# Kernel tuning notes

Hardware: AMD Instinct MI355X
Metric: run time of the kernel (lower is better)

The kernel has to match this reference:

```python
import jax, jax.numpy as jnp
import numpy as np

D_MODEL = 2048
N_HEADS = 16
D_HEAD = D_MODEL // N_HEADS


def setup_inputs() -> dict:
    key = jax.random.key(0)
    ks = jax.random.split(key, 9)
    s = 1.0 / np.sqrt(D_MODEL)
    x = jax.random.normal(ks[0], (2, 2048, D_MODEL), dtype=jnp.float32)
    wq = jax.random.uniform(ks[1], (D_MODEL, D_MODEL), jnp.float32, -s, s)
    wk = jax.random.uniform(ks[2], (D_MODEL, D_MODEL), jnp.float32, -s, s)
    wv = jax.random.uniform(ks[3], (D_MODEL, D_MODEL), jnp.float32, -s, s)
    wo = jax.random.uniform(ks[4], (D_MODEL, D_MODEL), jnp.float32, -s, s)
    bq = jax.random.uniform(ks[5], (D_MODEL,), jnp.float32, -s, s)
    bk = jax.random.uniform(ks[6], (D_MODEL,), jnp.float32, -s, s)
    bv = jax.random.uniform(ks[7], (D_MODEL,), jnp.float32, -s, s)
    bo = jax.random.uniform(ks[8], (D_MODEL,), jnp.float32, -s, s)
    return {"x": x, "wq": wq, "bq": bq, "wk": wk, "bk": bk,
            "wv": wv, "bv": bv, "wo": wo, "bo": bo}


def reference(x, wq, bq, wk, bk, wv, bv, wo, bo):
    b, s, _ = x.shape
    # torch Linear: y = x @ W.T + b
    q = (jnp.einsum('bsd,ed->bse', x, wq) + bq).reshape(b, s, N_HEADS, D_HEAD)
    k = (jnp.einsum('bsd,ed->bse', x, wk) + bk).reshape(b, s, N_HEADS, D_HEAD)
    v = (jnp.einsum('bsd,ed->bse', x, wv) + bv).reshape(b, s, N_HEADS, D_HEAD)
    scale = 1.0 / np.sqrt(D_HEAD).astype(np.float32)
    # [b, h, s, s] attention scores (naive full materialization, as in source)
    attn = jnp.einsum('bqhd,bkhd->bhqk', q, k) * scale
    attn = jax.nn.softmax(attn, axis=-1)
    out = jnp.einsum('bhqk,bkhd->bqhd', attn, v).reshape(b, s, D_MODEL)
    return jnp.einsum('bsd,ed->bse', out, wo) + bo
```

## Files before the change

kernel.cpp:

```cpp
#include <hip/hip_runtime.h>

#define D_MODEL 2048
#define SEQ     2048
#define NB      2
#define NH      16
#define DH      128
#define MROWS   (NB*SEQ)
#define GK      2048
#define NT      (GK/64)

typedef __bf16 bf16x8 __attribute__((ext_vector_type(8)));
typedef float  f32x4  __attribute__((ext_vector_type(4)));
typedef unsigned short ushort8 __attribute__((ext_vector_type(8)));
typedef unsigned int   u32x4   __attribute__((ext_vector_type(4)));

__device__ __forceinline__ unsigned short f2bf(float f) {
  unsigned int u = __float_as_uint(f);
  u += 0x7FFFu + ((u >> 16) & 1u);
  return (unsigned short)(u >> 16);
}

__device__ __forceinline__ unsigned int cvtpk_bf16(float lo, float hi) {
  unsigned int r;
  asm("v_cvt_pk_bf16_f32 %0, %1, %2" : "=v"(r) : "v"(lo), "v"(hi));
  return r;
}

__device__ __forceinline__ void gload16(void* lds, const void* g) {
  __builtin_amdgcn_global_load_lds(
      (__attribute__((address_space(1))) void*)(g),
      (__attribute__((address_space(3))) void*)(lds), 16, 0, 0);
}

__global__ __launch_bounds__(256) void cast_f32_bf16(
    const float* __restrict__ in, unsigned short* __restrict__ out) {
  int i = blockIdx.x * 256 + threadIdx.x;
  const float4* p = (const float4*)in;
  float4 a = p[2*i], b = p[2*i+1];
  ushort8 o;
  o[0]=f2bf(a.x); o[1]=f2bf(a.y); o[2]=f2bf(a.z); o[3]=f2bf(a.w);
  o[4]=f2bf(b.x); o[5]=f2bf(b.y); o[6]=f2bf(b.z); o[7]=f2bf(b.w);
  ((ushort8*)out)[i] = o;
}

__global__ __launch_bounds__(512, 2) void gemm256(
    const unsigned short* __restrict__ A,
    const unsigned short* __restrict__ B,
    const float* __restrict__ b0, const float* __restrict__ b1,
    const float* __restrict__ b2,
    unsigned short* __restrict__ qo, unsigned short* __restrict__ ko,
    unsigned short* __restrict__ vo, float* __restrict__ fo,
    int mode, int nblk)
{
  __shared__ char lds[3*49152];

  const int tid  = threadIdx.x;
  const int lane = tid & 63, wid = tid >> 6;
  const int la   = lane & 15, hi = lane >> 4;
  const int wm   = wid >> 2,  wn = wid & 3;

  const int linear = ((int)(blockIdx.x & 7)) * (nblk >> 3) + ((int)blockIdx.x >> 3);
  const int bm = linear & 31, bn = linear >> 5;

  const unsigned short* Ab = A + (size_t)(bm*128) * GK;
  const unsigned short* Bb = B + (size_t)(bn*256) * GK;

  f32x4 acc[4][4];
  #pragma unroll
  for (int m = 0; m < 4; m++)
    #pragma unroll
    for (int n = 0; n < 4; n++) acc[m][n] = f32x4{0.f,0.f,0.f,0.f};

#define STAGE_A(slot, kt) do {                                                \
    int sb_ = (slot) * 49152;                                                 \
    _Pragma("unroll")                                                         \
    for (int j = 0; j < 2; j++) {                                             \
      int idx = j*512 + tid;                                                  \
      int row = idx >> 3;                                                     \
      int c   = (idx & 7) << 4;                                               \
      gload16(lds + sb_ + idx*16,                                             \
              Ab + (size_t)row*GK + (kt)*64 + ((c ^ ((row&7)<<4)) >> 1));     \
    }                                                                         \
  } while (0)

#define STAGE_B(slot, kt) do {                                                \
    int sb_ = (slot) * 49152;                                                 \
    _Pragma("unroll")                                                         \
    for (int j = 0; j < 4; j++) {                                             \
      int idx = j*512 + tid;                                                  \
      int row = idx >> 3;                                                     \
      int c   = (idx & 7) << 4;                                               \
      gload16(lds + sb_ + 16384 + idx*16,                                     \
              Bb + (size_t)row*GK + (kt)*64 + ((c ^ ((row&7)<<4)) >> 1));     \
    }                                                                         \
  } while (0)

  STAGE_A(0, 0); STAGE_B(0, 0);
  STAGE_A(1, 1); STAGE_B(1, 1);

  int cs = 0, ps = 2;
  const int xr = (la & 7) << 4;

  #pragma unroll 1
  for (int t = 0; t < NT; ++t) {
    if (t + 1 < NT) asm volatile("s_waitcnt vmcnt(6)" ::: "memory");
    else            asm volatile("s_waitcnt vmcnt(0)" ::: "memory");
    __builtin_amdgcn_s_barrier();

    const char* sa  = lds + cs*49152;
    const char* sbp = sa + 16384;

    bf16x8 bfr[4][2], aA[2][2];
    #pragma unroll
    for (int n = 0; n < 4; n++)
      #pragma unroll
      for (int ks = 0; ks < 2; ks++)
        bfr[n][ks] = *(const bf16x8*)(sbp + (((wn*64 + n*16 + la)*128 + ks*64 + hi*16) ^ xr));
    #pragma unroll
    for (int m = 0; m < 2; m++)
      #pragma unroll
      for (int ks = 0; ks < 2; ks++)
        aA[m][ks] = *(const bf16x8*)(sa + (((wm*64 + m*16 + la)*128 + ks*64 + hi*16) ^ xr));

    if (t + 2 < NT) STAGE_A(ps, t + 2);

    asm volatile("s_waitcnt lgkmcnt(0)" ::: "memory");
    __builtin_amdgcn_sched_barrier(0);
    __builtin_amdgcn_s_setprio(1);
    #pragma unroll
    for (int m = 0; m < 2; m++)
      #pragma unroll
      for (int n = 0; n < 4; n++)
        #pragma unroll
        for (int ks = 0; ks < 2; ks++)
          acc[m][n] = __builtin_amdgcn_mfma_f32_16x16x32_bf16(aA[m][ks], bfr[n][ks], acc[m][n], 0, 0, 0);
    __builtin_amdgcn_s_setprio(0);
    __builtin_amdgcn_s_barrier();

    bf16x8 aB[2][2];
    #pragma unroll
    for (int m = 0; m < 2; m++)
      #pragma unroll
      for (int ks = 0; ks < 2; ks++)
        aB[m][ks] = *(const bf16x8*)(sa + (((wm*64 + (m+2)*16 + la)*128 + ks*64 + hi*16) ^ xr));

    if (t + 2 < NT) STAGE_B(ps, t + 2);

    asm volatile("s_waitcnt lgkmcnt(0)" ::: "memory");
    __builtin_amdgcn_sched_barrier(0);
    __builtin_amdgcn_s_setprio(1);
    #pragma unroll
    for (int m = 0; m < 2; m++)
      #pragma unroll
      for (int n = 0; n < 4; n++)
        #pragma unroll
        for (int ks = 0; ks < 2; ks++)
          acc[m+2][n] = __builtin_amdgcn_mfma_f32_16x16x32_bf16(aB[m][ks], bfr[n][ks], acc[m+2][n], 0, 0, 0);
    __builtin_amdgcn_s_setprio(0);

    cs = cs + 1; if (cs == 3) cs = 0;
    ps = ps + 1; if (ps == 3) ps = 0;
  }
#undef STAGE_A
#undef STAGE_B

  const int row0 = bm*128 + wm*64;
  const int col0 = bn*256 + wn*64;

  if (mode == 1) {
    #pragma unroll
    for (int n = 0; n < 4; n++) {
      int col = col0 + n*16 + la;
      float bv = b0[col];
      #pragma unroll
      for (int m = 0; m < 4; m++)
        #pragma unroll
        for (int r = 0; r < 4; r++) {
          int row = row0 + m*16 + hi*4 + r;
          fo[(size_t)row*D_MODEL + col] = acc[m][n][r] + bv;
        }
    }
  } else {
    const int mat = col0 >> 11;
    const float* bp = (mat == 0) ? b0 : (mat == 1) ? b1 : b2;
    #pragma unroll
    for (int n = 0; n < 4; n++) {
      int col = col0 + n*16 + la;
      int c   = col & 2047;
      int h   = c >> 7, d = c & 127;
      float bv = bp[c];
      #pragma unroll
      for (int m = 0; m < 4; m++)
        #pragma unroll
        for (int r = 0; r < 4; r++) {
          int row = row0 + m*16 + hi*4 + r;
          int b   = row >> 11, s = row & (SEQ-1);
          unsigned short val = f2bf(acc[m][n][r] + bv);
          if (mat == 0) {
            qo[((size_t)(b*NH + h)*SEQ + s)*DH + d] = val;
          } else if (mat == 1) {
            size_t base = ((size_t)(b*NH + h)*SEQ + (size_t)(s >> 6)*64)*DH;
            int boff = (((s & 63) << 8) + (d << 1)) ^ ((s & 7) << 4);
            ko[base + (boff >> 1)] = val;
          } else {
            size_t base = ((size_t)(b*NH + h)*SEQ + (size_t)(s >> 6)*64)*DH;
            int boff = ((d << 7) + ((s & 63) << 1)) ^ ((d & 7) << 4);
            vo[base + (boff >> 1)] = val;
          }
        }
    }
  }
}

__global__ __launch_bounds__(256, 2) void attn_fwd(
    const unsigned short* __restrict__ Q,
    const unsigned short* __restrict__ Kg,
    const unsigned short* __restrict__ VTg,
    unsigned short* __restrict__ O)
{
  __shared__ unsigned short Ks [2][64*128];
  __shared__ unsigned short VTs[2][128*64];

  const int tid  = threadIdx.x;
  const int lane = tid & 63, wid = tid >> 6;
  const int la   = lane & 15, hi = lane >> 4;
  const int swz  = ((int)(blockIdx.x & 7) << 6) + ((int)blockIdx.x >> 3);
  const int bh   = swz >> 4;
  const int q0   = (swz & 15) << 7;
  const int b    = bh >> 4, h = bh & 15;

  const unsigned short* Qh = Q   + (size_t)bh * SEQ * DH;
  const unsigned short* Kh = Kg  + (size_t)bh * SEQ * DH;
  const unsigned short* Vh = VTg + (size_t)bh * SEQ * DH;

  const int qrow = q0 + wid * 32;

  bf16x8 qf[2][4];
  #pragma unroll
  for (int qi = 0; qi < 2; qi++)
    #pragma unroll
    for (int ks = 0; ks < 4; ks++)
      qf[qi][ks] = *(const bf16x8*)(Qh + (size_t)(qrow + qi*16 + la)*DH + ks*32 + hi*8);

  f32x4 o[2][8];
  float mrun[2], lrun[2];
  #pragma unroll
  for (int qi = 0; qi < 2; qi++) {
    #pragma unroll
    for (int df = 0; df < 8; df++) o[qi][df] = f32x4{0.f,0.f,0.f,0.f};
    mrun[qi] = -1e30f; lrun[qi] = 0.f;
  }

  #pragma unroll
  for (int i = 0; i < 4; i++) {
    int off = i*4096 + tid*16;
    gload16((char*)Ks[0]  + off, (const char*)Kh + off);
    gload16((char*)VTs[0] + off, (const char*)Vh + off);
  }
  __syncthreads();

  const float sc = 0.08838834764831845f;

  #pragma unroll 1
  for (int t = 0; t < SEQ/64; ++t) {
    const int cur = t & 1;

    if (t + 1 < SEQ/64) {
      const char* kt = (const char*)(Kh + (size_t)(t+1)*(64*DH));
      const char* vt = (const char*)(Vh + (size_t)(t+1)*(64*DH));
      #pragma unroll
      for (int i = 0; i < 4; i++) {
        int off = i*4096 + tid*16;
        gload16((char*)Ks[cur^1]  + off, kt + off);
        gload16((char*)VTs[cur^1] + off, vt + off);
      }
    }

    f32x4 S[4][2];
    #pragma unroll
    for (int mf = 0; mf < 4; mf++)
      #pragma unroll
      for (int qi = 0; qi < 2; qi++) S[mf][qi] = f32x4{0.f,0.f,0.f,0.f};
    #pragma unroll
    for (int ks = 0; ks < 4; ks++) {
      bf16x8 kf[4];
      #pragma unroll
      for (int mf = 0; mf < 4; mf++) {
        int boff = (((mf*16 + la) << 8) + (ks << 6) + (hi << 4)) ^ ((la & 7) << 4);
        kf[mf] = *(const bf16x8*)((const char*)Ks[cur] + boff);
      }
      #pragma unroll
      for (int mf = 0; mf < 4; mf++)
        #pragma unroll
        for (int qi = 0; qi < 2; qi++)
          S[mf][qi] = __builtin_amdgcn_mfma_f32_16x16x32_bf16(kf[mf], qf[qi][ks], S[mf][qi], 0, 0, 0);
    }

    unsigned int pf[2][2][4];
    #pragma unroll
    for (int qi = 0; qi < 2; qi++) {
      float pm = S[0][qi][0];
      #pragma unroll
      for (int mf = 0; mf < 4; mf++)
        #pragma unroll
        for (int r = 0; r < 4; r++) pm = fmaxf(pm, S[mf][qi][r]);
      pm = fmaxf(pm, __shfl_xor(pm, 16));
      pm = fmaxf(pm, __shfl_xor(pm, 32));
      pm *= sc;
      float mn    = fmaxf(mrun[qi], pm);
      float alpha = __expf(mrun[qi] - mn);
      mrun[qi] = mn;

      float p[4][4]; float rs = 0.f;
      #pragma unroll
      for (int mf = 0; mf < 4; mf++)
        #pragma unroll
        for (int r = 0; r < 4; r++) {
          float e = __expf(fmaf(S[mf][qi][r], sc, -mn));
          p[mf][r] = e; rs += e;
        }
      rs += __shfl_xor(rs, 16);
      rs += __shfl_xor(rs, 32);
      lrun[qi] = lrun[qi]*alpha + rs;

      #pragma unroll
      for (int r = 0; r < 4; r++) {
        float ar = __shfl(alpha, (lane & 48) | ((hi << 2) | r), 64);
        #pragma unroll
        for (int df = 0; df < 8; df++) o[qi][df][r] *= ar;
      }

      unsigned int c[4][2];
      #pragma unroll
      for (int mf = 0; mf < 4; mf++) {
        c[mf][0] = cvtpk_bf16(p[mf][0], p[mf][1]);
        c[mf][1] = cvtpk_bf16(p[mf][2], p[mf][3]);
      }
      #pragma unroll
      for (int ks2 = 0; ks2 < 2; ks2++) {
        #pragma unroll
        for (int w = 0; w < 4; w++) {
          int src = la + 16*(2*(hi & 1) + (w >> 1));
          unsigned int t0 = __shfl(c[2*ks2    ][w & 1], src, 64);
          unsigned int t1 = __shfl(c[2*ks2 + 1][w & 1], src, 64);
          pf[qi][ks2][w] = (hi >> 1) ? t1 : t0;
        }
      }
    }

    #pragma unroll
    for (int ks2 = 0; ks2 < 2; ks2++) {
      #pragma unroll
      for (int df = 0; df < 8; df++) {
        int vrow = df*16 + la;
        int boff = ((vrow << 7) + (ks2 << 6) + (hi << 4)) ^ ((la & 7) << 4);
        bf16x8 vf = *(const bf16x8*)((const char*)VTs[cur] + boff);
        #pragma unroll
        for (int qi = 0; qi < 2; qi++) {
          u32x4 pw = {pf[qi][ks2][0], pf[qi][ks2][1], pf[qi][ks2][2], pf[qi][ks2][3]};
          o[qi][df] = __builtin_amdgcn_mfma_f32_16x16x32_bf16(
              __builtin_bit_cast(bf16x8, pw), vf, o[qi][df], 0, 0, 0);
        }
      }
    }
    __syncthreads();
  }

  unsigned short* Ob = O + (size_t)b * SEQ * D_MODEL + h * DH;
  #pragma unroll
  for (int qi = 0; qi < 2; qi++) {
    float linv[4];
    #pragma unroll
    for (int r = 0; r < 4; r++)
      linv[r] = 1.0f / __shfl(lrun[qi], (lane & 48) | ((hi << 2) | r), 64);
    #pragma unroll
    for (int df = 0; df < 8; df++)
      #pragma unroll
      for (int r = 0; r < 4; r++) {
        int srow = qrow + qi*16 + hi*4 + r;
        Ob[(size_t)srow * D_MODEL + df*16 + la] = f2bf(o[qi][df][r] * linv[r]);
      }
  }
}

extern "C" void kernel_launch(void* const* d_in, const int* in_sizes, int n_in,
                              void* d_out, int out_size, void* d_ws, size_t ws_size,
                              hipStream_t stream) {
  const float* x  = (const float*)d_in[0];
  const float* wq = (const float*)d_in[1];
  const float* bq = (const float*)d_in[2];
  const float* wk = (const float*)d_in[3];
  const float* bk = (const float*)d_in[4];
  const float* wv = (const float*)d_in[5];
  const float* bv = (const float*)d_in[6];
  const float* wo = (const float*)d_in[7];
  const float* bo = (const float*)d_in[8];
  float* out = (float*)d_out;

  const size_t X = (size_t)MROWS * D_MODEL;
  const size_t W = (size_t)D_MODEL * D_MODEL;

  unsigned short* ws  = (unsigned short*)d_ws;
  unsigned short* xb  = ws;
  unsigned short* wqb = xb  + X;
  unsigned short* wkb = wqb + W;
  unsigned short* wvb = wkb + W;
  unsigned short* wob = wvb + W;
  unsigned short* qb  = wob + W;
  unsigned short* kb  = qb  + X;
  unsigned short* vtg = kb  + X;
  unsigned short* ab  = vtg + X;

  cast_f32_bf16<<<dim3((unsigned)(X/2048)), 256, 0, stream>>>(x,  xb);
  cast_f32_bf16<<<dim3((unsigned)(W/2048)), 256, 0, stream>>>(wq, wqb);
  cast_f32_bf16<<<dim3((unsigned)(W/2048)), 256, 0, stream>>>(wk, wkb);
  cast_f32_bf16<<<dim3((unsigned)(W/2048)), 256, 0, stream>>>(wv, wvb);
  cast_f32_bf16<<<dim3((unsigned)(W/2048)), 256, 0, stream>>>(wo, wob);

  gemm256<<<dim3(768), 512, 0, stream>>>(xb, wqb, bq, bk, bv,
                                         qb, kb, vtg, nullptr, 0, 768);

  attn_fwd<<<dim3(512), 256, 0, stream>>>(qb, kb, vtg, ab);

  gemm256<<<dim3(256), 512, 0, stream>>>(ab, wob, bo, bo, bo,
                                         nullptr, nullptr, nullptr, out, 1, 256);
}
```

Before: 301.1 us.

## Use a dedicated 256x256-tile QKV GEMM and fuse the four weight casts

```diff
diff --git a/kernel.cpp b/kernel.cpp
--- a/kernel.cpp
+++ b/kernel.cpp
@@ -43,14 +43,138 @@
   ((ushort8*)out)[i] = o;
 }
 
+__global__ __launch_bounds__(256) void cast_w4(
+    const float* __restrict__ w0, const float* __restrict__ w1,
+    const float* __restrict__ w2, const float* __restrict__ w3,
+    unsigned short* __restrict__ out) {
+  int gb = blockIdx.x;
+  int which = gb >> 11;
+  const float* src = (which == 0) ? w0 : (which == 1) ? w1 : (which == 2) ? w2 : w3;
+  int i = (gb & 2047) * 256 + threadIdx.x;
+  const float4* p = (const float4*)src;
+  float4 a = p[2*i], b = p[2*i+1];
+  ushort8 o;
+  o[0]=f2bf(a.x); o[1]=f2bf(a.y); o[2]=f2bf(a.z); o[3]=f2bf(a.w);
+  o[4]=f2bf(b.x); o[5]=f2bf(b.y); o[6]=f2bf(b.z); o[7]=f2bf(b.w);
+  ((ushort8*)out)[(size_t)which * 524288 + i] = o;
+}
+
+__global__ __launch_bounds__(512, 2) void gemmq(
+    const unsigned short* __restrict__ A,
+    const unsigned short* __restrict__ Bw,
+    const float* __restrict__ b0, const float* __restrict__ b1,
+    const float* __restrict__ b2,
+    unsigned short* __restrict__ qo, unsigned short* __restrict__ ko,
+    unsigned short* __restrict__ vo)
+{
+  __shared__ char lds[2*65536];
+
+  const int tid  = threadIdx.x;
+  const int lane = tid & 63, wid = tid >> 6;
+  const int la   = lane & 15, hi = lane >> 4;
+  const int wm   = wid >> 2,  wn = wid & 3;
+
+  const int xcd = (int)blockIdx.x & 7, ii = (int)blockIdx.x >> 3;
+  const int bm  = ii & 15;
+  const int bn  = xcd * 3 + (ii >> 4);
+
+  const unsigned short* Ab = A  + (size_t)(bm*256) * GK;
+  const unsigned short* Bb = Bw + (size_t)(bn*256) * GK;
+
+  f32x4 acc[8][4];
+  #pragma unroll
+  for (int m = 0; m < 8; m++)
+    #pragma unroll
+    for (int n = 0; n < 4; n++) acc[m][n] = f32x4{0.f,0.f,0.f,0.f};
+
+#define STG(slot, kt) do {                                                    \
+    char* base_ = lds + (slot)*65536;                                         \
+    _Pragma("unroll")                                                         \
+    for (int j = 0; j < 4; j++) {                                             \
+      int idx = j*512 + tid;                                                  \
+      int row = idx >> 3;                                                     \
+      int c   = (idx & 7) << 4;                                               \
+      int se  = ((c ^ ((row&7)<<4)) >> 1);                                    \
+      gload16(base_ + idx*16,         Ab + (size_t)row*GK + (kt)*64 + se);    \
+      gload16(base_ + 32768 + idx*16, Bb + (size_t)row*GK + (kt)*64 + se);    \
+    }                                                                         \
+  } while (0)
+
+  STG(0, 0);
+  const int xr = (la & 7) << 4;
+
+  #pragma unroll 1
+  for (int t = 0; t < NT; ++t) {
+    if (t + 1 < NT) {
+      STG((t+1)&1, t+1);
+      asm volatile("s_waitcnt vmcnt(8)" ::: "memory");
+    } else {
+      asm volatile("s_waitcnt vmcnt(0)" ::: "memory");
+    }
+    __builtin_amdgcn_s_barrier();
+
+    const char* sa = lds + (t&1)*65536;
+    const char* sb = sa + 32768;
+
+    #pragma unroll
+    for (int ks = 0; ks < 2; ks++) {
+      bf16x8 a[8], b[4];
+      #pragma unroll
+      for (int m = 0; m < 8; m++)
+        a[m] = *(const bf16x8*)(sa + (((wm*128 + m*16 + la)*128 + ks*64 + hi*16) ^ xr));
+      #pragma unroll
+      for (int n = 0; n < 4; n++)
+        b[n] = *(const bf16x8*)(sb + (((wn*64 + n*16 + la)*128 + ks*64 + hi*16) ^ xr));
+      asm volatile("s_waitcnt lgkmcnt(0)" ::: "memory");
+      __builtin_amdgcn_sched_barrier(0);
+      __builtin_amdgcn_s_setprio(1);
+      #pragma unroll
+      for (int m = 0; m < 8; m++)
+        #pragma unroll
+        for (int n = 0; n < 4; n++)
+          acc[m][n] = __builtin_amdgcn_mfma_f32_16x16x32_bf16(a[m], b[n], acc[m][n], 0, 0, 0);
+      __builtin_amdgcn_s_setprio(0);
+      __builtin_amdgcn_s_barrier();
+    }
+  }
+#undef STG
+
+  const int mat = bn >> 3;
+  const float* bp = (mat == 0) ? b0 : (mat == 1) ? b1 : b2;
+  #pragma unroll
+  for (int n = 0; n < 4; n++) {
+    int col = bn*256 + wn*64 + n*16 + la;
+    int c   = col & 2047;
+    int h   = c >> 7, d = c & 127;
+    float bv = bp[c];
+    #pragma unroll
+    for (int m = 0; m < 8; m++)
+      #pragma unroll
+      for (int r = 0; r < 4; r++) {
+        int row = bm*256 + wm*128 + m*16 + hi*4 + r;
+        int bb  = row >> 11, s = row & (SEQ-1);
+        unsigned short val = f2bf(acc[m][n][r] + bv);
+        if (mat == 0) {
+          qo[((size_t)(bb*NH + h)*SEQ + s)*DH + d] = val;
+        } else if (mat == 1) {
+          size_t base = ((size_t)(bb*NH + h)*SEQ + (size_t)(s >> 6)*64)*DH;
+          int boff = (((s & 63) << 8) + (d << 1)) ^ ((s & 7) << 4);
+          ko[base + (boff >> 1)] = val;
+        } else {
+          size_t base = ((size_t)(bb*NH + h)*SEQ + (size_t)(s >> 6)*64)*DH;
+          int boff = ((d << 7) + ((s & 63) << 1)) ^ ((d & 7) << 4);
+          vo[base + (boff >> 1)] = val;
+        }
+      }
+  }
+}
+
 __global__ __launch_bounds__(512, 2) void gemm256(
     const unsigned short* __restrict__ A,
     const unsigned short* __restrict__ B,
-    const float* __restrict__ b0, const float* __restrict__ b1,
-    const float* __restrict__ b2,
-    unsigned short* __restrict__ qo, unsigned short* __restrict__ ko,
-    unsigned short* __restrict__ vo, float* __restrict__ fo,
-    int mode, int nblk)
+    const float* __restrict__ b0,
+    float* __restrict__ fo,
+    int nblk)
 {
   __shared__ char lds[3*49152];
 
@@ -166,49 +290,17 @@
 
   const int row0 = bm*128 + wm*64;
   const int col0 = bn*256 + wn*64;
-
-  if (mode == 1) {
-    #pragma unroll
-    for (int n = 0; n < 4; n++) {
-      int col = col0 + n*16 + la;
-      float bv = b0[col];
-      #pragma unroll
-      for (int m = 0; m < 4; m++)
-        #pragma unroll
-        for (int r = 0; r < 4; r++) {
-          int row = row0 + m*16 + hi*4 + r;
-          fo[(size_t)row*D_MODEL + col] = acc[m][n][r] + bv;
-        }
-    }
-  } else {
-    const int mat = col0 >> 11;
-    const float* bp = (mat == 0) ? b0 : (mat == 1) ? b1 : b2;
-    #pragma unroll
-    for (int n = 0; n < 4; n++) {
-      int col = col0 + n*16 + la;
-      int c   = col & 2047;
-      int h   = c >> 7, d = c & 127;
-      float bv = bp[c];
-      #pragma unroll
-      for (int m = 0; m < 4; m++)
-        #pragma unroll
-        for (int r = 0; r < 4; r++) {
-          int row = row0 + m*16 + hi*4 + r;
-          int b   = row >> 11, s = row & (SEQ-1);
-          unsigned short val = f2bf(acc[m][n][r] + bv);
-          if (mat == 0) {
-            qo[((size_t)(b*NH + h)*SEQ + s)*DH + d] = val;
-          } else if (mat == 1) {
-            size_t base = ((size_t)(b*NH + h)*SEQ + (size_t)(s >> 6)*64)*DH;
-            int boff = (((s & 63) << 8) + (d << 1)) ^ ((s & 7) << 4);
-            ko[base + (boff >> 1)] = val;
-          } else {
-            size_t base = ((size_t)(b*NH + h)*SEQ + (size_t)(s >> 6)*64)*DH;
-            int boff = ((d << 7) + ((s & 63) << 1)) ^ ((d & 7) << 4);
-            vo[base + (boff >> 1)] = val;
-          }
-        }
-    }
+  #pragma unroll
+  for (int n = 0; n < 4; n++) {
+    int col = col0 + n*16 + la;
+    float bv = b0[col];
+    #pragma unroll
+    for (int m = 0; m < 4; m++)
+      #pragma unroll
+      for (int r = 0; r < 4; r++) {
+        int row = row0 + m*16 + hi*4 + r;
+        fo[(size_t)row*D_MODEL + col] = acc[m][n][r] + bv;
+      }
   }
 }
 
@@ -411,17 +503,12 @@
   unsigned short* vtg = kb  + X;
   unsigned short* ab  = vtg + X;
 
-  cast_f32_bf16<<<dim3((unsigned)(X/2048)), 256, 0, stream>>>(x,  xb);
-  cast_f32_bf16<<<dim3((unsigned)(W/2048)), 256, 0, stream>>>(wq, wqb);
-  cast_f32_bf16<<<dim3((unsigned)(W/2048)), 256, 0, stream>>>(wk, wkb);
-  cast_f32_bf16<<<dim3((unsigned)(W/2048)), 256, 0, stream>>>(wv, wvb);
-  cast_f32_bf16<<<dim3((unsigned)(W/2048)), 256, 0, stream>>>(wo, wob);
-
-  gemm256<<<dim3(768), 512, 0, stream>>>(xb, wqb, bq, bk, bv,
-                                         qb, kb, vtg, nullptr, 0, 768);
+  cast_f32_bf16<<<dim3((unsigned)(X/2048)), 256, 0, stream>>>(x, xb);
+  cast_w4<<<dim3(8192), 256, 0, stream>>>(wq, wk, wv, wo, wqb);
+
+  gemmq<<<dim3(384), 512, 0, stream>>>(xb, wqb, bq, bk, bv, qb, kb, vtg);
 
   attn_fwd<<<dim3(512), 256, 0, stream>>>(qb, kb, vtg, ab);
 
-  gemm256<<<dim3(256), 512, 0, stream>>>(ab, wob, bo, bo, bo,
-                                         nullptr, nullptr, nullptr, out, 1, 256);
-}
+  gemm256<<<dim3(256), 512, 0, stream>>>(ab, wob, bo, out, 256);
+}
```

Measured after the change: 321.8 us. +6.9%, slower.

## Shrink GEMM tile to 128x128 with double buffering and batch weight casts

Applied to the files above, without the earlier changes.

```diff
diff --git a/kernel.cpp b/kernel.cpp
--- a/kernel.cpp
+++ b/kernel.cpp
@@ -43,7 +43,23 @@
   ((ushort8*)out)[i] = o;
 }
 
-__global__ __launch_bounds__(512, 2) void gemm256(
+__global__ __launch_bounds__(256) void cast_w4(
+    const float* __restrict__ w0, const float* __restrict__ w1,
+    const float* __restrict__ w2, const float* __restrict__ w3,
+    unsigned short* __restrict__ out) {
+  int gb = blockIdx.x;
+  int which = gb >> 11;
+  const float* src = (which == 0) ? w0 : (which == 1) ? w1 : (which == 2) ? w2 : w3;
+  int i = (gb & 2047) * 256 + threadIdx.x;
+  const float4* p = (const float4*)src;
+  float4 a = p[2*i], b = p[2*i+1];
+  ushort8 o;
+  o[0]=f2bf(a.x); o[1]=f2bf(a.y); o[2]=f2bf(a.z); o[3]=f2bf(a.w);
+  o[4]=f2bf(b.x); o[5]=f2bf(b.y); o[6]=f2bf(b.z); o[7]=f2bf(b.w);
+  ((ushort8*)out)[(size_t)which * 524288 + i] = o;
+}
+
+__global__ __launch_bounds__(256, 2) void gemm128(
     const unsigned short* __restrict__ A,
     const unsigned short* __restrict__ B,
     const float* __restrict__ b0, const float* __restrict__ b1,
@@ -52,18 +68,18 @@
     unsigned short* __restrict__ vo, float* __restrict__ fo,
     int mode, int nblk)
 {
-  __shared__ char lds[3*49152];
+  __shared__ char lds[2*32768];
 
   const int tid  = threadIdx.x;
   const int lane = tid & 63, wid = tid >> 6;
   const int la   = lane & 15, hi = lane >> 4;
-  const int wm   = wid >> 2,  wn = wid & 3;
+  const int wm   = wid >> 1,  wn = wid & 1;
 
   const int linear = ((int)(blockIdx.x & 7)) * (nblk >> 3) + ((int)blockIdx.x >> 3);
   const int bm = linear & 31, bn = linear >> 5;
 
   const unsigned short* Ab = A + (size_t)(bm*128) * GK;
-  const unsigned short* Bb = B + (size_t)(bn*256) * GK;
+  const unsigned short* Bb = B + (size_t)(bn*128) * GK;
 
   f32x4 acc[4][4];
   #pragma unroll
@@ -71,58 +87,46 @@
     #pragma unroll
     for (int n = 0; n < 4; n++) acc[m][n] = f32x4{0.f,0.f,0.f,0.f};
 
-#define STAGE_A(slot, kt) do {                                                \
-    int sb_ = (slot) * 49152;                                                 \
+#define STG(slot, kt) do {                                                    \
+    char* base_ = lds + (slot)*32768;                                         \
     _Pragma("unroll")                                                         \
-    for (int j = 0; j < 2; j++) {                                             \
-      int idx = j*512 + tid;                                                  \
+    for (int j = 0; j < 4; j++) {                                             \
+      int idx = j*256 + tid;                                                  \
       int row = idx >> 3;                                                     \
       int c   = (idx & 7) << 4;                                               \
-      gload16(lds + sb_ + idx*16,                                             \
-              Ab + (size_t)row*GK + (kt)*64 + ((c ^ ((row&7)<<4)) >> 1));     \
+      int se  = ((c ^ ((row&7)<<4)) >> 1);                                    \
+      gload16(base_ + idx*16,         Ab + (size_t)row*GK + (kt)*64 + se);    \
+      gload16(base_ + 16384 + idx*16, Bb + (size_t)row*GK + (kt)*64 + se);    \
     }                                                                         \
   } while (0)
 
-#define STAGE_B(slot, kt) do {                                                \
-    int sb_ = (slot) * 49152;                                                 \
-    _Pragma("unroll")                                                         \
-    for (int j = 0; j < 4; j++) {                                             \
-      int idx = j*512 + tid;                                                  \
-      int row = idx >> 3;                                                     \
-      int c   = (idx & 7) << 4;                                               \
-      gload16(lds + sb_ + 16384 + idx*16,                                     \
-              Bb + (size_t)row*GK + (kt)*64 + ((c ^ ((row&7)<<4)) >> 1));     \
-    }                                                                         \
-  } while (0)
-
-  STAGE_A(0, 0); STAGE_B(0, 0);
-  STAGE_A(1, 1); STAGE_B(1, 1);
-
-  int cs = 0, ps = 2;
+  STG(0, 0);
   const int xr = (la & 7) << 4;
 
   #pragma unroll 1
   for (int t = 0; t < NT; ++t) {
-    if (t + 1 < NT) asm volatile("s_waitcnt vmcnt(6)" ::: "memory");
-    else            asm volatile("s_waitcnt vmcnt(0)" ::: "memory");
+    if (t + 1 < NT) {
+      STG((t+1)&1, t+1);
+      asm volatile("s_waitcnt vmcnt(8)" ::: "memory");
+    } else {
+      asm volatile("s_waitcnt vmcnt(0)" ::: "memory");
+    }
     __builtin_amdgcn_s_barrier();
 
-    const char* sa  = lds + cs*49152;
-    const char* sbp = sa + 16384;
+    const char* sa = lds + (t&1)*32768;
+    const char* sb = sa + 16384;
 
     bf16x8 bfr[4][2], aA[2][2];
     #pragma unroll
     for (int n = 0; n < 4; n++)
       #pragma unroll
       for (int ks = 0; ks < 2; ks++)
-        bfr[n][ks] = *(const bf16x8*)(sbp + (((wn*64 + n*16 + la)*128 + ks*64 + hi*16) ^ xr));
+        bfr[n][ks] = *(const bf16x8*)(sb + (((wn*64 + n*16 + la)*128 + ks*64 + hi*16) ^ xr));
     #pragma unroll
     for (int m = 0; m < 2; m++)
       #pragma unroll
       for (int ks = 0; ks < 2; ks++)
         aA[m][ks] = *(const bf16x8*)(sa + (((wm*64 + m*16 + la)*128 + ks*64 + hi*16) ^ xr));
-
-    if (t + 2 < NT) STAGE_A(ps, t + 2);
 
     asm volatile("s_waitcnt lgkmcnt(0)" ::: "memory");
     __builtin_amdgcn_sched_barrier(0);
@@ -144,8 +148,6 @@
       for (int ks = 0; ks < 2; ks++)
         aB[m][ks] = *(const bf16x8*)(sa + (((wm*64 + (m+2)*16 + la)*128 + ks*64 + hi*16) ^ xr));
 
-    if (t + 2 < NT) STAGE_B(ps, t + 2);
-
     asm volatile("s_waitcnt lgkmcnt(0)" ::: "memory");
     __builtin_amdgcn_sched_barrier(0);
     __builtin_amdgcn_s_setprio(1);
@@ -157,15 +159,12 @@
         for (int ks = 0; ks < 2; ks++)
           acc[m+2][n] = __builtin_amdgcn_mfma_f32_16x16x32_bf16(aB[m][ks], bfr[n][ks], acc[m+2][n], 0, 0, 0);
     __builtin_amdgcn_s_setprio(0);
-
-    cs = cs + 1; if (cs == 3) cs = 0;
-    ps = ps + 1; if (ps == 3) ps = 0;
-  }
-#undef STAGE_A
-#undef STAGE_B
+    __builtin_amdgcn_s_barrier();
+  }
+#undef STG
 
   const int row0 = bm*128 + wm*64;
-  const int col0 = bn*256 + wn*64;
+  const int col0 = bn*128 + wn*64;
 
   if (mode == 1) {
     #pragma unroll
@@ -194,16 +193,16 @@
         #pragma unroll
         for (int r = 0; r < 4; r++) {
           int row = row0 + m*16 + hi*4 + r;
-          int b   = row >> 11, s = row & (SEQ-1);
+          int bb  = row >> 11, s = row & (SEQ-1);
           unsigned short val = f2bf(acc[m][n][r] + bv);
           if (mat == 0) {
-            qo[((size_t)(b*NH + h)*SEQ + s)*DH + d] = val;
+            qo[((size_t)(bb*NH + h)*SEQ + s)*DH + d] = val;
           } else if (mat == 1) {
-            size_t base = ((size_t)(b*NH + h)*SEQ + (size_t)(s >> 6)*64)*DH;
+            size_t base = ((size_t)(bb*NH + h)*SEQ + (size_t)(s >> 6)*64)*DH;
             int boff = (((s & 63) << 8) + (d << 1)) ^ ((s & 7) << 4);
             ko[base + (boff >> 1)] = val;
           } else {
-            size_t base = ((size_t)(b*NH + h)*SEQ + (size_t)(s >> 6)*64)*DH;
+            size_t base = ((size_t)(bb*NH + h)*SEQ + (size_t)(s >> 6)*64)*DH;
             int boff = ((d << 7) + ((s & 63) << 1)) ^ ((d & 7) << 4);
             vo[base + (boff >> 1)] = val;
           }
@@ -411,17 +410,14 @@
   unsigned short* vtg = kb  + X;
   unsigned short* ab  = vtg + X;
 
-  cast_f32_bf16<<<dim3((unsigned)(X/2048)), 256, 0, stream>>>(x,  xb);
-  cast_f32_bf16<<<dim3((unsigned)(W/2048)), 256, 0, stream>>>(wq, wqb);
-  cast_f32_bf16<<<dim3((unsigned)(W/2048)), 256, 0, stream>>>(wk, wkb);
-  cast_f32_bf16<<<dim3((unsigned)(W/2048)), 256, 0, stream>>>(wv, wvb);
-  cast_f32_bf16<<<dim3((unsigned)(W/2048)), 256, 0, stream>>>(wo, wob);
-
-  gemm256<<<dim3(768), 512, 0, stream>>>(xb, wqb, bq, bk, bv,
-                                         qb, kb, vtg, nullptr, 0, 768);
+  cast_f32_bf16<<<dim3((unsigned)(X/2048)), 256, 0, stream>>>(x, xb);
+  cast_w4<<<dim3(8192), 256, 0, stream>>>(wq, wk, wv, wo, wqb);
+
+  gemm128<<<dim3(1536), 256, 0, stream>>>(xb, wqb, bq, bk, bv,
+                                          qb, kb, vtg, nullptr, 0, 1536);
 
   attn_fwd<<<dim3(512), 256, 0, stream>>>(qb, kb, vtg, ab);
 
-  gemm256<<<dim3(256), 512, 0, stream>>>(ab, wob, bo, bo, bo,
-                                         nullptr, nullptr, nullptr, out, 1, 256);
-}
+  gemm128<<<dim3(512), 256, 0, stream>>>(ab, wob, bo, bo, bo,
+                                         nullptr, nullptr, nullptr, out, 1, 512);
+}
```

Result: slower. 311.8 us (+3.6%).

## Use exp2 softmax with lazy rescaling and fuse weight casts into one launch

Applied to the files above, without the earlier changes.

```diff
diff --git a/kernel.cpp b/kernel.cpp
--- a/kernel.cpp
+++ b/kernel.cpp
@@ -41,6 +41,22 @@
   o[0]=f2bf(a.x); o[1]=f2bf(a.y); o[2]=f2bf(a.z); o[3]=f2bf(a.w);
   o[4]=f2bf(b.x); o[5]=f2bf(b.y); o[6]=f2bf(b.z); o[7]=f2bf(b.w);
   ((ushort8*)out)[i] = o;
+}
+
+__global__ __launch_bounds__(256) void cast_w4(
+    const float* __restrict__ w0, const float* __restrict__ w1,
+    const float* __restrict__ w2, const float* __restrict__ w3,
+    unsigned short* __restrict__ out) {
+  int gb = blockIdx.x;
+  int which = gb >> 11;
+  const float* src = (which == 0) ? w0 : (which == 1) ? w1 : (which == 2) ? w2 : w3;
+  int i = (gb & 2047) * 256 + threadIdx.x;
+  const float4* p = (const float4*)src;
+  float4 a = p[2*i], b = p[2*i+1];
+  ushort8 o;
+  o[0]=f2bf(a.x); o[1]=f2bf(a.y); o[2]=f2bf(a.z); o[3]=f2bf(a.w);
+  o[4]=f2bf(b.x); o[5]=f2bf(b.y); o[6]=f2bf(b.z); o[7]=f2bf(b.w);
+  ((ushort8*)out)[(size_t)which * 524288 + i] = o;
 }
 
 __global__ __launch_bounds__(512, 2) void gemm256(
@@ -194,16 +210,16 @@
         #pragma unroll
         for (int r = 0; r < 4; r++) {
           int row = row0 + m*16 + hi*4 + r;
-          int b   = row >> 11, s = row & (SEQ-1);
+          int bb  = row >> 11, s = row & (SEQ-1);
           unsigned short val = f2bf(acc[m][n][r] + bv);
           if (mat == 0) {
-            qo[((size_t)(b*NH + h)*SEQ + s)*DH + d] = val;
+            qo[((size_t)(bb*NH + h)*SEQ + s)*DH + d] = val;
           } else if (mat == 1) {
-            size_t base = ((size_t)(b*NH + h)*SEQ + (size_t)(s >> 6)*64)*DH;
+            size_t base = ((size_t)(bb*NH + h)*SEQ + (size_t)(s >> 6)*64)*DH;
             int boff = (((s & 63) << 8) + (d << 1)) ^ ((s & 7) << 4);
             ko[base + (boff >> 1)] = val;
           } else {
-            size_t base = ((size_t)(b*NH + h)*SEQ + (size_t)(s >> 6)*64)*DH;
+            size_t base = ((size_t)(bb*NH + h)*SEQ + (size_t)(s >> 6)*64)*DH;
             int boff = ((d << 7) + ((s & 63) << 1)) ^ ((d & 7) << 4);
             vo[base + (boff >> 1)] = val;
           }
@@ -259,7 +275,7 @@
   }
   __syncthreads();
 
-  const float sc = 0.08838834764831845f;
+  const float sc2 = 0.1275424483f;
 
   #pragma unroll 1
   for (int t = 0; t < SEQ/64; ++t) {
@@ -306,29 +322,35 @@
         for (int r = 0; r < 4; r++) pm = fmaxf(pm, S[mf][qi][r]);
       pm = fmaxf(pm, __shfl_xor(pm, 16));
       pm = fmaxf(pm, __shfl_xor(pm, 32));
-      pm *= sc;
-      float mn    = fmaxf(mrun[qi], pm);
-      float alpha = __expf(mrun[qi] - mn);
-      mrun[qi] = mn;
+      pm *= sc2;
+
+      float mn;
+      if (__all(pm <= mrun[qi] + 8.0f)) {
+        mn = mrun[qi];
+      } else {
+        mn = fmaxf(mrun[qi], pm);
+        float alpha = __builtin_amdgcn_exp2f(mrun[qi] - mn);
+        mrun[qi] = mn;
+        lrun[qi] *= alpha;
+        #pragma unroll
+        for (int r = 0; r < 4; r++) {
+          float ar = __shfl(alpha, (lane & 48) | ((hi << 2) | r), 64);
+          #pragma unroll
+          for (int df = 0; df < 8; df++) o[qi][df][r] *= ar;
+        }
+      }
 
       float p[4][4]; float rs = 0.f;
       #pragma unroll
       for (int mf = 0; mf < 4; mf++)
         #pragma unroll
         for (int r = 0; r < 4; r++) {
-          float e = __expf(fmaf(S[mf][qi][r], sc, -mn));
+          float e = __builtin_amdgcn_exp2f(fmaf(S[mf][qi][r], sc2, -mn));
           p[mf][r] = e; rs += e;
         }
       rs += __shfl_xor(rs, 16);
       rs += __shfl_xor(rs, 32);
-      lrun[qi] = lrun[qi]*alpha + rs;
-
-      #pragma unroll
-      for (int r = 0; r < 4; r++) {
-        float ar = __shfl(alpha, (lane & 48) | ((hi << 2) | r), 64);
-        #pragma unroll
-        for (int df = 0; df < 8; df++) o[qi][df][r] *= ar;
-      }
+      lrun[qi] += rs;
 
       unsigned int c[4][2];
       #pragma unroll
@@ -411,11 +433,8 @@
   unsigned short* vtg = kb  + X;
   unsigned short* ab  = vtg + X;
 
-  cast_f32_bf16<<<dim3((unsigned)(X/2048)), 256, 0, stream>>>(x,  xb);
-  cast_f32_bf16<<<dim3((unsigned)(W/2048)), 256, 0, stream>>>(wq, wqb);
-  cast_f32_bf16<<<dim3((unsigned)(W/2048)), 256, 0, stream>>>(wk, wkb);
-  cast_f32_bf16<<<dim3((unsigned)(W/2048)), 256, 0, stream>>>(wv, wvb);
-  cast_f32_bf16<<<dim3((unsigned)(W/2048)), 256, 0, stream>>>(wo, wob);
+  cast_f32_bf16<<<dim3((unsigned)(X/2048)), 256, 0, stream>>>(x, xb);
+  cast_w4<<<dim3(8192), 256, 0, stream>>>(wq, wk, wv, wo, wqb);
 
   gemm256<<<dim3(768), 512, 0, stream>>>(xb, wqb, bq, bk, bv,
                                          qb, kb, vtg, nullptr, 0, 768);
```

Result: faster. 284.9 us (-5.4%).
